# Optimization experiments

Hardware: AMD Instinct MI355X
Metric: run time of the kernel (lower is better)

The kernel has to match this reference:

```python
import jax, jax.numpy as jnp
import numpy as np

B, T, D_IN, H, D_ENC, P, D_ATT = 64, 20, 512, 512, 2048, 196, 512


def setup_inputs() -> dict:
    key = jax.random.key(0)
    ks = jax.random.split(key, 12)
    s = 0.05  # weight scale to keep gates out of saturation
    return {
        "x": jax.random.normal(ks[0], (B, T, D_IN), jnp.float32),
        "cnn_features": jax.random.normal(ks[1], (B, P, D_ENC), jnp.float32),
        "Wi": jax.random.normal(ks[2], (D_IN + H + D_ENC, H), jnp.float32) * s,
        "bi": jnp.zeros((H,), jnp.float32),
        "Wf": jax.random.normal(ks[3], (D_IN + H + D_ENC, H), jnp.float32) * s,
        "bf": jnp.zeros((H,), jnp.float32),
        "Wc": jax.random.normal(ks[4], (D_IN + H + D_ENC, H), jnp.float32) * s,
        "bc": jnp.zeros((H,), jnp.float32),
        "Wo": jax.random.normal(ks[5], (D_IN + H + D_ENC, H), jnp.float32) * s,
        "bo": jnp.zeros((H,), jnp.float32),
        "Wa_feat": jax.random.normal(ks[6], (D_ENC, D_ATT), jnp.float32) * s,
        "Wa_h": jax.random.normal(ks[7], (H, D_ATT), jnp.float32) * s,
        "ba": jnp.zeros((D_ATT,), jnp.float32),
        "v": jax.random.normal(ks[8], (D_ATT,), jnp.float32) * s,
    }


def reference(x, cnn_features, Wi, bi, Wf, bf, Wc, bc, Wo, bo, Wa_feat, Wa_h, ba, v):
    batch, seq_len, _ = x.shape
    hid = Wi.shape[1]
    # feature projection is h-independent: hoist out of the time loop
    feat_proj = jnp.einsum('bpe,ea->bpa', cnn_features, Wa_feat) + ba  # [B,P,A]

    def step(carry, x_t):
        h, c = carry
        # additive (Bahdanau) attention over pixels
        e = jnp.einsum('bpa,a->bp', jnp.tanh(feat_proj + (h @ Wa_h)[:, None, :]), v)
        alpha = jax.nn.softmax(e, axis=-1)                      # [B,P]
        ctx = jnp.einsum('bp,bpe->be', alpha, cnn_features)     # [B,E]
        comb = jnp.concatenate([x_t, h, ctx], axis=1)           # [B,D_IN+H+E]
        i_t = jax.nn.sigmoid(comb @ Wi + bi)
        f_t = jax.nn.sigmoid(comb @ Wf + bf)
        o_t = jax.nn.sigmoid(comb @ Wo + bo)
        c_tilde = jnp.tanh(comb @ Wc + bc)
        c_new = f_t * c + i_t * c_tilde
        h_new = o_t * jnp.tanh(c_new)
        return (h_new, c_new), h_new

    h0 = jnp.zeros((batch, hid), x.dtype)
    c0 = jnp.zeros((batch, hid), x.dtype)
    (h_T, c_T), ys = jax.lax.scan(step, (h0, c0), jnp.swapaxes(x, 0, 1))
    outputs = jnp.swapaxes(ys, 0, 1)  # [B,T,H]
    return outputs, h_T, c_T
```

## Files before the change

### kernel.cpp

```cpp
#include <hip/hip_runtime.h>

typedef unsigned short u16;
typedef unsigned int u32;
typedef __attribute__((ext_vector_type(8))) short bf16x8;
typedef __attribute__((ext_vector_type(4))) float f32x4;

#define NB 64
#define NT 20
#define NH 512
#define NP 196
#define NE 2048
#define NA 512

__device__ __forceinline__ u16 f2bf(float f) {
  u32 b = __float_as_uint(f);
  return (u16)((b + 0x7FFFu + ((b >> 16) & 1u)) >> 16);
}
__device__ __forceinline__ float bf2f(u16 u) { return __uint_as_float(((u32)u) << 16); }
__device__ __forceinline__ float tanh_fast(float x) {
  float xc = fminf(fmaxf(x, -15.f), 15.f);
  float e2 = __builtin_amdgcn_exp2f(xc * 2.885390082f);
  return (e2 - 1.f) * __builtin_amdgcn_rcpf(e2 + 1.f);
}
__device__ __forceinline__ float sigmoid_fast(float x) {
  return __builtin_amdgcn_rcpf(1.f + __builtin_amdgcn_exp2f(x * -1.44269504f));
}

__device__ __forceinline__ void gload_lds16(const u16* g, u16* l) {
  __builtin_amdgcn_global_load_lds((const __attribute__((address_space(1))) void*)g,
                                   (__attribute__((address_space(3))) void*)l, 16, 0, 0);
}

__global__ __launch_bounds__(256) void conv_bf16(const float4* __restrict__ src,
                                                 u16* __restrict__ dst, int n4) {
  int i = blockIdx.x * 256 + threadIdx.x;
  int stride = gridDim.x * 256;
  for (; i < n4; i += stride) {
    float4 v = src[i];
    u32 lo = (u32)f2bf(v.x) | ((u32)f2bf(v.y) << 16);
    u32 hi = (u32)f2bf(v.z) | ((u32)f2bf(v.w) << 16);
    *(uint2*)(dst + (size_t)i * 4) = make_uint2(lo, hi);
  }
}

__global__ __launch_bounds__(128) void conv_x(const float* __restrict__ x,
                                              u16* __restrict__ xbT) {
  int b = blockIdx.x, t = blockIdx.y, tid = threadIdx.x;
  float4 v = *(const float4*)(x + ((size_t)b * NT + t) * 512 + tid * 4);
  u32 lo = (u32)f2bf(v.x) | ((u32)f2bf(v.y) << 16);
  u32 hi = (u32)f2bf(v.z) | ((u32)f2bf(v.w) << 16);
  *(uint2*)(xbT + ((size_t)t * NB + b) * 512 + tid * 4) = make_uint2(lo, hi);
}

__global__ __launch_bounds__(256) void transpose_w(const float* __restrict__ W0,
                                                   const float* __restrict__ W1,
                                                   const float* __restrict__ W2,
                                                   const float* __restrict__ W3,
                                                   u16* __restrict__ dst, int row_off, int K) {
  const float* src = blockIdx.z == 0 ? W0 : blockIdx.z == 1 ? W1 : blockIdx.z == 2 ? W2 : W3;
  __shared__ float tile[32][33];
  int k0 = blockIdx.x * 32, n0 = blockIdx.y * 32;
  int tx = threadIdx.x & 31, ty = threadIdx.x >> 5;
#pragma unroll
  for (int i = 0; i < 4; ++i)
    tile[ty + i * 8][tx] = src[(size_t)(row_off + k0 + ty + i * 8) * 512 + n0 + tx];
  __syncthreads();
#pragma unroll
  for (int i = 0; i < 4; ++i) {
    int n = n0 + ty + i * 8, k = k0 + tx;
    dst[((size_t)blockIdx.z * 512 + n) * K + k] = f2bf(tile[tx][ty + i * 8]);
  }
}

__global__ __launch_bounds__(256) void gemm_bf16(const u16* __restrict__ A,
                                                 const u16* __restrict__ BT,
                                                 float* __restrict__ C, int M, int N, int K) {
  __shared__ u16 lA[128 * 64];
  __shared__ u16 lB[128 * 64];
  const int tid = threadIdx.x;
  const int lane = tid & 63;
  const int wid = tid >> 6;
  const int m0 = blockIdx.x * 128, n0 = blockIdx.y * 128;
  const int wm = (wid >> 1) * 64, wn = (wid & 1) * 64;
  f32x4 acc[4][4] = {};

  const int cbase = wid * 256;
  int srcr[4], srcc[4];
#pragma unroll
  for (int it = 0; it < 4; ++it) {
    int c = cbase + it * 64 + lane;
    srcr[it] = c >> 3;
    srcc[it] = ((c & 7) ^ ((c >> 3) & 7)) * 8;
  }

  for (int k0 = 0; k0 < K; k0 += 64) {
    __syncthreads();
#pragma unroll
    for (int it = 0; it < 4; ++it) {
      gload_lds16(A + (size_t)(m0 + srcr[it]) * K + k0 + srcc[it],
                  lA + (size_t)(cbase + it * 64) * 8);
      gload_lds16(BT + (size_t)(n0 + srcr[it]) * K + k0 + srcc[it],
                  lB + (size_t)(cbase + it * 64) * 8);
    }
    __syncthreads();
#pragma unroll
    for (int kk = 0; kk < 2; ++kk) {
      int kchunk = kk * 4 + (lane >> 4);
      bf16x8 af[4], bg[4];
#pragma unroll
      for (int i = 0; i < 4; ++i) {
        int row = wm + i * 16 + (lane & 15);
        af[i] = *(const bf16x8*)(lA + row * 64 + ((kchunk ^ (row & 7)) * 8));
        int rowb = wn + i * 16 + (lane & 15);
        bg[i] = *(const bf16x8*)(lB + rowb * 64 + ((kchunk ^ (rowb & 7)) * 8));
      }
#pragma unroll
      for (int i = 0; i < 4; ++i)
#pragma unroll
        for (int j = 0; j < 4; ++j)
          acc[i][j] = __builtin_amdgcn_mfma_f32_16x16x32_bf16(af[i], bg[j], acc[i][j], 0, 0, 0);
    }
  }
#pragma unroll
  for (int i = 0; i < 4; ++i) {
    int m = m0 + wm + i * 16 + ((lane >> 4) * 4);
#pragma unroll
    for (int j = 0; j < 4; ++j) {
      int n = n0 + wn + j * 16 + (lane & 15);
#pragma unroll
      for (int r = 0; r < 4; ++r) C[(size_t)(m + r) * N + n] = acc[i][j][r];
    }
  }
}

__global__ __launch_bounds__(512, 2) void gemm256(const u16* __restrict__ A,
                                                  const u16* __restrict__ BT,
                                                  const float* __restrict__ bias,
                                                  u16* __restrict__ fpb, u16* __restrict__ cnW,
                                                  int K, int grid_n) {
  __shared__ u16 lA[256 * 64];
  __shared__ u16 lB[256 * 64];
  const int tid = threadIdx.x;
  const int lane = tid & 63;
  const int wid = tid >> 6;
  const int nblk = gridDim.x;
  const int q = nblk >> 3, rr = nblk & 7;
  const int xcd = blockIdx.x & 7, jj = blockIdx.x >> 3;
  const int swz = (xcd < rr ? xcd * (q + 1) : rr * (q + 1) + (xcd - rr) * q) + jj;
  const int mt = swz / grid_n, nt = swz - mt * grid_n;
  const int m0 = mt * 256, n0 = nt * 256;
  const int wm = (wid >> 2) * 128, wn = (wid & 3) * 64;
  f32x4 acc[8][4] = {};

  const int cbase = wid * 64;
  int srcr[4], srcc[4];
#pragma unroll
  for (int it = 0; it < 4; ++it) {
    int c = it * 512 + cbase + lane;
    srcr[it] = c >> 3;
    srcc[it] = ((c & 7) ^ ((c >> 3) & 7)) * 8;
  }

  for (int k0 = 0; k0 < K; k0 += 64) {
    __syncthreads();
#pragma unroll
    for (int it = 0; it < 4; ++it) {
      int ldso = (it * 512 + cbase) * 8;
      gload_lds16(A + (size_t)(m0 + srcr[it]) * K + k0 + srcc[it], lA + ldso);
      gload_lds16(BT + (size_t)(n0 + srcr[it]) * K + k0 + srcc[it], lB + ldso);
    }
    __syncthreads();
#pragma unroll
    for (int kk = 0; kk < 2; ++kk) {
      int kchunk = kk * 4 + (lane >> 4);
      bf16x8 af[8], bg[4];
#pragma unroll
      for (int i = 0; i < 8; ++i) {
        int row = wm + i * 16 + (lane & 15);
        af[i] = *(const bf16x8*)(lA + row * 64 + ((kchunk ^ (row & 7)) * 8));
      }
#pragma unroll
      for (int j = 0; j < 4; ++j) {
        int rowb = wn + j * 16 + (lane & 15);
        bg[j] = *(const bf16x8*)(lB + rowb * 64 + ((kchunk ^ (rowb & 7)) * 8));
      }
#pragma unroll
      for (int i = 0; i < 8; ++i)
#pragma unroll
        for (int j = 0; j < 4; ++j)
          acc[i][j] = __builtin_amdgcn_mfma_f32_16x16x32_bf16(af[i], bg[j], acc[i][j], 0, 0, 0);
    }
  }

#pragma unroll
  for (int i = 0; i < 8; ++i) {
    int m = m0 + wm + i * 16 + ((lane >> 4) * 4);
#pragma unroll
    for (int j = 0; j < 4; ++j) {
      int n = n0 + wn + j * 16 + (lane & 15);
      float bv = (n < 512) ? bias[n] : 0.f;
#pragma unroll
      for (int r = 0; r < 4; ++r) {
        float val = acc[i][j][r] + bv;
        u32 me = (u32)(m + r);
        if (n < 512) {
          fpb[(size_t)me * 512 + n] = f2bf(val);
        } else {
          u32 bdx = me / 196u;
          u32 p = me - bdx * 196u;
          u32 g = (u32)(n - 512) >> 9;
          u32 n9 = (u32)(n - 512) & 511u;
          cnW[(((size_t)bdx * 4 + g) * 196 + p) * 512 + n9] = f2bf(val);
        }
      }
    }
  }
}

__global__ __launch_bounds__(256) void hproj(const u16* __restrict__ hprev,
                                             const u16* __restrict__ wcT,
                                             float* __restrict__ hp) {
  const int ntile = blockIdx.x;
  const int tid = threadIdx.x, lane = tid & 63, kh = tid >> 6;
  const int l15 = lane & 15;
  const u16* Bp = wcT + (size_t)(ntile * 16 + l15) * 512 + kh * 128 + ((lane >> 4) * 8);
  const u16* Ap = hprev + (size_t)l15 * 512 + kh * 128 + ((lane >> 4) * 8);
  f32x4 acc[4] = {};
#pragma unroll
  for (int ks = 0; ks < 4; ++ks) {
    bf16x8 bb = *(const bf16x8*)(Bp + ks * 32);
#pragma unroll
    for (int mf = 0; mf < 4; ++mf) {
      bf16x8 a = *(const bf16x8*)(Ap + (size_t)mf * 16 * 512 + ks * 32);
      acc[mf] = __builtin_amdgcn_mfma_f32_16x16x32_bf16(a, bb, acc[mf], 0, 0, 0);
    }
  }
  __shared__ float pre[4][64][16];
  const int rrow = (lane >> 4) * 4;
#pragma unroll
  for (int mf = 0; mf < 4; ++mf)
#pragma unroll
    for (int r = 0; r < 4; ++r) pre[kh][mf * 16 + rrow + r][l15] = acc[mf][r];
  __syncthreads();
  const int m = tid >> 2, n = (tid & 3) * 4;
  float4 s;
  float* sp = (float*)&s;
#pragma unroll
  for (int j = 0; j < 4; ++j)
    sp[j] = pre[0][m][n + j] + pre[1][m][n + j] + pre[2][m][n + j] + pre[3][m][n + j];
  *(float4*)(hp + (size_t)m * 2560 + ntile * 16 + n) = s;
}

__global__ __launch_bounds__(1024) void attn_gates(
    const u16* __restrict__ fpb, const float* __restrict__ hp, const float* __restrict__ v,
    const u16* __restrict__ cw, const float* __restrict__ xw, const float* __restrict__ bi,
    const float* __restrict__ bfg, const float* __restrict__ bc, const float* __restrict__ bo,
    float* __restrict__ cbuf, float* __restrict__ out, u16* __restrict__ hnext, int t) {
  const int b = blockIdx.x & 63;
  const int half = blockIdx.x >> 6;
  const int tid = threadIdx.x;
  const int lane = tid & 63, wid = tid >> 6;
  __shared__ float smem_a[1024];
  __shared__ float sm[16];
  __shared__ float alp[200];
  __shared__ float red[8192];

  float* hwa = smem_a;
  float* vv = smem_a + 512;
  if (tid < 512) {
    hwa[tid] = (t > 0) ? hp[(size_t)b * 2560 + 2048 + tid] : 0.f;
    vv[tid] = v[tid];
  }
  if (tid >= 196 && tid < 256) red[tid] = -3e38f;
  __syncthreads();

  float hw[8], vr[8];
#pragma unroll
  for (int j = 0; j < 8; ++j) {
    hw[j] = hwa[lane * 8 + j];
    vr[j] = vv[lane * 8 + j];
  }
  for (int p = wid; p < NP; p += 16) {
    const u16* fp = fpb + ((size_t)b * NP + p) * 512 + lane * 8;
    uint4 raw = *(const uint4*)fp;
    u32 w[4] = {raw.x, raw.y, raw.z, raw.w};
    float part = 0.f;
#pragma unroll
    for (int j = 0; j < 8; ++j) {
      u16 u = (u16)(w[j >> 1] >> ((j & 1) * 16));
      part += tanh_fast(bf2f(u) + hw[j]) * vr[j];
    }
#pragma unroll
    for (int off = 32; off > 0; off >>= 1) part += __shfl_xor(part, off);
    if (lane == 0) red[p] = part;
  }
  __syncthreads();

  float ev = 0.f, w = 0.f;
  if (tid < 256) {
    ev = red[tid];
    float m_ = ev;
#pragma unroll
    for (int off = 32; off > 0; off >>= 1) m_ = fmaxf(m_, __shfl_xor(m_, off));
    if (lane == 0) sm[wid] = m_;
  }
  __syncthreads();
  if (tid < 256) {
    float mx = fmaxf(fmaxf(sm[0], sm[1]), fmaxf(sm[2], sm[3]));
    w = (tid < NP) ? __builtin_amdgcn_exp2f((ev - mx) * 1.44269504f) : 0.f;
    float s_ = w;
#pragma unroll
    for (int off = 32; off > 0; off >>= 1) s_ += __shfl_xor(s_, off);
    if (lane == 0) sm[8 + wid] = s_;
  }
  __syncthreads();
  if (tid < NP) {
    float tot = (sm[8] + sm[9]) + (sm[10] + sm[11]);
    alp[tid] = w * __builtin_amdgcn_rcpf(tot);
  }
  __syncthreads();

  {
    const int g = tid >> 8, pg = (tid >> 5) & 7, colc = tid & 31;
    const u16* base = cw + ((size_t)(b * 4 + g) * 196) * 512 + half * 256 + colc * 8;
    float acc[8] = {};
    for (int i = 0; i < 25; ++i) {
      int p = pg + i * 8;
      if (p < NP) {
        float al = alp[p];
        uint4 raw = *(const uint4*)(base + (size_t)p * 512);
        u32 wds[4] = {raw.x, raw.y, raw.z, raw.w};
#pragma unroll
        for (int j = 0; j < 8; ++j) acc[j] += al * bf2f((u16)(wds[j >> 1] >> ((j & 1) * 16)));
      }
    }
#pragma unroll
    for (int j = 0; j < 8; ++j) red[((g * 8 + pg) * 32 + colc) * 8 + j] = acc[j];
  }
  __syncthreads();

  float* pre4 = smem_a;
  {
    const int g = tid >> 8, nn = tid & 255;
    float s = 0.f;
#pragma unroll
    for (int pg = 0; pg < 8; ++pg) s += red[((g * 8 + pg) * 32 + (nn >> 3)) * 8 + (nn & 7)];
    pre4[g * 256 + nn] = s;
  }
  __syncthreads();

  if (tid < 256) {
    const int ng = half * 256 + tid;
    const size_t xwo = ((size_t)t * NB + b) * 2048;
    const size_t hpb = (size_t)b * 2560;
    float hwh0 = 0.f, hwh1 = 0.f, hwh2 = 0.f, hwh3 = 0.f;
    if (t > 0) {
      hwh0 = hp[hpb + ng];
      hwh1 = hp[hpb + 512 + ng];
      hwh2 = hp[hpb + 1024 + ng];
      hwh3 = hp[hpb + 1536 + ng];
    }
    float ip = pre4[0 * 256 + tid] + xw[xwo + ng] + hwh0 + bi[ng];
    float fp = pre4[1 * 256 + tid] + xw[xwo + 512 + ng] + hwh1 + bfg[ng];
    float cp = pre4[2 * 256 + tid] + xw[xwo + 1024 + ng] + hwh2 + bc[ng];
    float op = pre4[3 * 256 + tid] + xw[xwo + 1536 + ng] + hwh3 + bo[ng];
    float it = sigmoid_fast(ip), ft = sigmoid_fast(fp), ot = sigmoid_fast(op);
    float ctl = tanh_fast(cp);
    float cold = (t > 0) ? cbuf[(size_t)b * 512 + ng] : 0.f;
    float cn = ft * cold + it * ctl;
    float hn = ot * tanh_fast(cn);
    cbuf[(size_t)b * 512 + ng] = cn;
    hnext[(size_t)b * 512 + ng] = f2bf(hn);
    out[((size_t)b * NT + t) * 512 + ng] = hn;
    if (t == NT - 1) {
      out[(size_t)NB * NT * 512 + (size_t)b * 512 + ng] = hn;
      out[(size_t)NB * NT * 512 + (size_t)NB * 512 + (size_t)b * 512 + ng] = cn;
    }
  }
}

extern "C" void kernel_launch(void* const* d_in, const int* in_sizes, int n_in, void* d_out,
                              int out_size, void* d_ws, size_t ws_size, hipStream_t stream) {
  const float* x = (const float*)d_in[0];
  const float* cnn = (const float*)d_in[1];
  const float* Wi = (const float*)d_in[2];
  const float* bi = (const float*)d_in[3];
  const float* Wf = (const float*)d_in[4];
  const float* bfv = (const float*)d_in[5];
  const float* Wc = (const float*)d_in[6];
  const float* bc = (const float*)d_in[7];
  const float* Wo = (const float*)d_in[8];
  const float* bo = (const float*)d_in[9];
  const float* Waf = (const float*)d_in[10];
  const float* Wah = (const float*)d_in[11];
  const float* ba = (const float*)d_in[12];
  const float* v = (const float*)d_in[13];
  float* out = (float*)d_out;

  char* base = (char*)d_ws;
  size_t off = 0;
  auto alloc = [&](size_t bytes) {
    char* r = base + off;
    off += (bytes + 255) & ~(size_t)255;
    return r;
  };
  u16* cnnb = (u16*)alloc((size_t)NB * NP * NE * 2);
  u16* fpb = (u16*)alloc((size_t)NB * NP * NA * 2);
  u16* cnW = (u16*)alloc((size_t)NB * 4 * NP * 512 * 2);
  u16* wbig = (u16*)alloc((size_t)2560 * 2048 * 2);
  u16* wcombT = (u16*)alloc((size_t)2560 * 512 * 2);
  u16* wxt = (u16*)alloc((size_t)4 * 512 * 512 * 2);
  u16* xbT = (u16*)alloc((size_t)NT * NB * 512 * 2);
  float* xw = (float*)alloc((size_t)NT * NB * 2048 * 4);
  u16* hbuf = (u16*)alloc((size_t)2 * NB * 512 * 2);
  float* cbuf = (float*)alloc((size_t)NB * 512 * 4);
  float* hp = (float*)alloc((size_t)NB * 2560 * 4);

  (void)ws_size;
  (void)in_sizes;
  (void)n_in;
  (void)out_size;

  conv_bf16<<<2048, 256, 0, stream>>>((const float4*)cnn, cnnb, (NB * NP * NE) / 4);
  conv_x<<<dim3(NB, NT), 128, 0, stream>>>(x, xbT);
  {
    dim3 g1(512 / 32, 16, 4);
    transpose_w<<<g1, 256, 0, stream>>>(Wi, Wf, Wc, Wo, wxt, 0, 512);
    dim3 g2(2048 / 32, 16, 1);
    transpose_w<<<g2, 256, 0, stream>>>(Waf, Waf, Waf, Waf, wbig, 0, 2048);
    dim3 g3(2048 / 32, 16, 4);
    transpose_w<<<g3, 256, 0, stream>>>(Wi, Wf, Wc, Wo, wbig + (size_t)512 * 2048, 1024, 2048);
    dim3 g4(512 / 32, 16, 4);
    transpose_w<<<g4, 256, 0, stream>>>(Wi, Wf, Wc, Wo, wcombT, 512, 512);
    dim3 g5(512 / 32, 16, 1);
    transpose_w<<<g5, 256, 0, stream>>>(Wah, Wah, Wah, Wah, wcombT + (size_t)2048 * 512, 0, 512);
  }

  gemm256<<<49 * 10, 512, 0, stream>>>(cnnb, wbig, ba, fpb, cnW, 2048, 10);

  {
    dim3 g(1280 / 128, 2048 / 128);
    gemm_bf16<<<g, 256, 0, stream>>>(xbT, wxt, xw, 1280, 2048, 512);
  }

  for (int t = 0; t < NT; ++t) {
    const u16* hprev = hbuf + (size_t)(t & 1) * NB * 512;
    u16* hnext = hbuf + (size_t)((t + 1) & 1) * NB * 512;
    if (t > 0) hproj<<<160, 256, 0, stream>>>(hprev, wcombT, hp);
    attn_gates<<<128, 1024, 0, stream>>>(fpb, hp, v, cnW, xw, bi, bfv, bc, bo, cbuf, out, hnext,
                                         t);
  }
}
```

Measured before the change: 706.6 us.

## Double-buffer gemm256 LDS and split K-tile into four interleaved MFMA phases

Rewrites the 256x256 bf16 GEMM main loop to use a double-buffered LDS tile. The global-to-LDS loads for the next K tile are issued in four quarter phases, interleaved with the MFMA work on the current tile, gated by explicit vmcnt waits, barriers and s_setprio. Each wave's output tile is remapped into four 64x32 quadrants so that each phase covers one quadrant of the accumulator. The aim is to hide global load latency behind compute. The cost is twice the LDS per block (128 KB), which may limit occupancy to one block per CU, and fragile manual waitcnt accounting.

```diff
diff --git a/kernel.cpp b/kernel.cpp
--- a/kernel.cpp
+++ b/kernel.cpp
@@ -29,6 +29,14 @@
 __device__ __forceinline__ void gload_lds16(const u16* g, u16* l) {
   __builtin_amdgcn_global_load_lds((const __attribute__((address_space(1))) void*)g,
                                    (__attribute__((address_space(3))) void*)l, 16, 0, 0);
+}
+
+template <int N>
+__device__ __forceinline__ void vwait() {
+  if constexpr (N >= 0)
+    asm volatile("s_waitcnt vmcnt(%0)" ::"i"(N) : "memory");
+  else
+    asm volatile("" ::: "memory");
 }
 
 __global__ __launch_bounds__(256) void conv_bf16(const float4* __restrict__ src,
@@ -133,71 +141,111 @@
   }
 }
 
+#define PHASE(MH, NH, CUR, DOSTAGE, MATB, HH, K1, WN)                                     \
+  do {                                                                                    \
+    const u16* pA_ = lds + (CUR) * 32768;                                                 \
+    const u16* pB_ = pA_ + 16384;                                                         \
+    bf16x8 af_[2][4], bg_[2][2];                                                          \
+    _Pragma("unroll") for (int kh_ = 0; kh_ < 2; ++kh_) {                                 \
+      const int kc_ = kh_ * 4 + (lane >> 4);                                              \
+      _Pragma("unroll") for (int i_ = 0; i_ < 4; ++i_) {                                  \
+        const int rw_ = (MH) * 128 + wmB + i_ * 16 + l15;                                 \
+        af_[kh_][i_] = *(const bf16x8*)(pA_ + rw_ * 64 + ((kc_ ^ (rw_ & 7)) * 8));        \
+      }                                                                                   \
+      _Pragma("unroll") for (int j_ = 0; j_ < 2; ++j_) {                                  \
+        const int rw_ = (NH) * 128 + wnB + j_ * 16 + l15;                                 \
+        bg_[kh_][j_] = *(const bf16x8*)(pB_ + rw_ * 64 + ((kc_ ^ (rw_ & 7)) * 8));        \
+      }                                                                                   \
+    }                                                                                     \
+    if (DOSTAGE) {                                                                        \
+      const u16* gsrc_ = (MATB) ? BT : A;                                                 \
+      const int r0_ = (MATB) ? n0 : m0;                                                   \
+      u16* ldst_ = lds + (1 - (CUR)) * 32768 + (MATB) * 16384;                            \
+      _Pragma("unroll") for (int s_ = 0; s_ < 2; ++s_)                                    \
+          gload_lds16(gsrc_ + (size_t)(r0_ + srcR[HH][s_]) * K + (K1) + srcC[HH][s_],     \
+                      ldst_ + ldsOff[HH][s_]);                                            \
+    }                                                                                     \
+    vwait<WN>();                                                                          \
+    __builtin_amdgcn_s_barrier();                                                         \
+    __builtin_amdgcn_s_setprio(1);                                                        \
+    _Pragma("unroll") for (int kh_ = 0; kh_ < 2; ++kh_)                                   \
+      _Pragma("unroll") for (int i_ = 0; i_ < 4; ++i_)                                    \
+        _Pragma("unroll") for (int j_ = 0; j_ < 2; ++j_)                                  \
+          acc[(MH) * 4 + i_][(NH) * 2 + j_] = __builtin_amdgcn_mfma_f32_16x16x32_bf16(    \
+              af_[kh_][i_], bg_[kh_][j_], acc[(MH) * 4 + i_][(NH) * 2 + j_], 0, 0, 0);    \
+    __builtin_amdgcn_s_setprio(0);                                                        \
+    __builtin_amdgcn_s_barrier();                                                         \
+  } while (0)
+
 __global__ __launch_bounds__(512, 2) void gemm256(const u16* __restrict__ A,
                                                   const u16* __restrict__ BT,
                                                   const float* __restrict__ bias,
                                                   u16* __restrict__ fpb, u16* __restrict__ cnW,
                                                   int K, int grid_n) {
-  __shared__ u16 lA[256 * 64];
-  __shared__ u16 lB[256 * 64];
+  __shared__ u16 lds[65536];
   const int tid = threadIdx.x;
   const int lane = tid & 63;
   const int wid = tid >> 6;
+  const int l15 = lane & 15;
   const int nblk = gridDim.x;
   const int q = nblk >> 3, rr = nblk & 7;
   const int xcd = blockIdx.x & 7, jj = blockIdx.x >> 3;
   const int swz = (xcd < rr ? xcd * (q + 1) : rr * (q + 1) + (xcd - rr) * q) + jj;
   const int mt = swz / grid_n, nt = swz - mt * grid_n;
   const int m0 = mt * 256, n0 = nt * 256;
-  const int wm = (wid >> 2) * 128, wn = (wid & 3) * 64;
+  const int wmB = (wid >> 2) * 64;
+  const int wnB = (wid & 3) * 32;
   f32x4 acc[8][4] = {};
 
-  const int cbase = wid * 64;
-  int srcr[4], srcc[4];
-#pragma unroll
-  for (int it = 0; it < 4; ++it) {
-    int c = it * 512 + cbase + lane;
-    srcr[it] = c >> 3;
-    srcc[it] = ((c & 7) ^ ((c >> 3) & 7)) * 8;
-  }
-
-  for (int k0 = 0; k0 < K; k0 += 64) {
-    __syncthreads();
-#pragma unroll
-    for (int it = 0; it < 4; ++it) {
-      int ldso = (it * 512 + cbase) * 8;
-      gload_lds16(A + (size_t)(m0 + srcr[it]) * K + k0 + srcc[it], lA + ldso);
-      gload_lds16(BT + (size_t)(n0 + srcr[it]) * K + k0 + srcc[it], lB + ldso);
-    }
-    __syncthreads();
-#pragma unroll
-    for (int kk = 0; kk < 2; ++kk) {
-      int kchunk = kk * 4 + (lane >> 4);
-      bf16x8 af[8], bg[4];
-#pragma unroll
-      for (int i = 0; i < 8; ++i) {
-        int row = wm + i * 16 + (lane & 15);
-        af[i] = *(const bf16x8*)(lA + row * 64 + ((kchunk ^ (row & 7)) * 8));
-      }
-#pragma unroll
-      for (int j = 0; j < 4; ++j) {
-        int rowb = wn + j * 16 + (lane & 15);
-        bg[j] = *(const bf16x8*)(lB + rowb * 64 + ((kchunk ^ (rowb & 7)) * 8));
-      }
-#pragma unroll
-      for (int i = 0; i < 8; ++i)
-#pragma unroll
-        for (int j = 0; j < 4; ++j)
-          acc[i][j] = __builtin_amdgcn_mfma_f32_16x16x32_bf16(af[i], bg[j], acc[i][j], 0, 0, 0);
-    }
+  int srcR[2][2], srcC[2][2], ldsOff[2][2];
+#pragma unroll
+  for (int h = 0; h < 2; ++h)
+#pragma unroll
+    for (int s = 0; s < 2; ++s) {
+      int c = h * 1024 + s * 512 + wid * 64 + lane;
+      srcR[h][s] = c >> 3;
+      srcC[h][s] = ((c & 7) ^ ((c >> 3) & 7)) * 8;
+      ldsOff[h][s] = (h * 1024 + s * 512 + wid * 64) * 8;
+    }
+
+#pragma unroll
+  for (int s = 0; s < 2; ++s)
+    gload_lds16(A + (size_t)(m0 + srcR[0][s]) * K + srcC[0][s], lds + ldsOff[0][s]);
+#pragma unroll
+  for (int s = 0; s < 2; ++s)
+    gload_lds16(BT + (size_t)(n0 + srcR[0][s]) * K + srcC[0][s], lds + 16384 + ldsOff[0][s]);
+#pragma unroll
+  for (int s = 0; s < 2; ++s)
+    gload_lds16(A + (size_t)(m0 + srcR[1][s]) * K + srcC[1][s], lds + ldsOff[1][s]);
+#pragma unroll
+  for (int s = 0; s < 2; ++s)
+    gload_lds16(BT + (size_t)(n0 + srcR[1][s]) * K + srcC[1][s], lds + 16384 + ldsOff[1][s]);
+  vwait<4>();
+  __builtin_amdgcn_s_barrier();
+
+  const int KT = K >> 6;
+  for (int kt = 0; kt < KT - 1; ++kt) {
+    const int cur = kt & 1;
+    const int k1 = (kt + 1) << 6;
+    PHASE(0, 0, cur, 1, 0, 0, k1, 4);
+    PHASE(1, 0, cur, 1, 1, 0, k1, 4);
+    PHASE(0, 1, cur, 1, 0, 1, k1, -1);
+    PHASE(1, 1, cur, 1, 1, 1, k1, 4);
+  }
+  {
+    const int cur = (KT - 1) & 1;
+    PHASE(0, 0, cur, 0, 0, 0, 0, 2);
+    PHASE(1, 0, cur, 0, 0, 0, 0, 0);
+    PHASE(0, 1, cur, 0, 0, 0, 0, -1);
+    PHASE(1, 1, cur, 0, 0, 0, 0, -1);
   }
 
 #pragma unroll
   for (int i = 0; i < 8; ++i) {
-    int m = m0 + wm + i * 16 + ((lane >> 4) * 4);
+    int m = m0 + (i >> 2) * 128 + wmB + (i & 3) * 16 + ((lane >> 4) * 4);
 #pragma unroll
     for (int j = 0; j < 4; ++j) {
-      int n = n0 + wn + j * 16 + (lane & 15);
+      int n = n0 + (j >> 1) * 128 + wnB + (j & 1) * 16 + l15;
       float bv = (n < 512) ? bias[n] : 0.f;
 #pragma unroll
       for (int r = 0; r < 4; ++r) {
```

After: 694.3 us. Within noise of the previous version (-1.7%).
